# Performance work log

Hardware: AMD Instinct MI355X
Metric: run time of the kernel (lower is better)

Reference implementation:

```python
import jax, jax.numpy as jnp
import numpy as np

B, N, C, H = 4, 4096, 1024, 16
HD = C // H  # head_dim = 64
EPS = 1e-6


def setup_inputs() -> dict:
    key = jax.random.key(0)
    ks = jax.random.split(key, 5)
    x = jax.random.normal(ks[0], (B, N, C), dtype=jnp.float32)
    s_in = 1.0 / np.sqrt(C)
    W_qkv = jax.random.normal(ks[1], (C, 3 * C), dtype=jnp.float32) * s_in
    b_qkv = jnp.zeros((3 * C,), dtype=jnp.float32)
    W_out = jax.random.normal(ks[2], (C, C), dtype=jnp.float32) * s_in
    b_out = jnp.zeros((C,), dtype=jnp.float32)
    return {"x": x, "W_qkv": W_qkv, "b_qkv": b_qkv, "W_out": W_out, "b_out": b_out}


def reference(x, W_qkv, b_qkv, W_out, b_out):
    # qkv projection: (B, N, 3C)
    qkv = jnp.einsum('bnc,cf->bnf', x, W_qkv) + b_qkv
    # rearrange 'b n (h d) -> b h n d' with d = 3*head_dim, then chunk into q,k,v
    qkv = qkv.reshape(B, N, H, 3 * HD).transpose(0, 2, 1, 3)  # (B,H,N,3*HD)
    q, k, v = jnp.split(qkv, 3, axis=-1)  # each (B,H,N,HD)
    # silu feature map
    q = jax.nn.silu(q)
    k = jax.nn.silu(k)
    # linear attention: state = k^T @ v per head  -> (B,H,HD,HD)
    state = jnp.einsum('bhnd,bhne->bhde', k, v)
    k_sum = k.sum(axis=2)  # (B,H,HD)
    num = jnp.einsum('bhnd,bhde->bhne', q, state)  # (B,H,N,HD)
    den = jnp.einsum('bhnd,bhd->bhn', q, k_sum)[..., None]  # (B,H,N,1)
    out = num / (den + EPS)
    # 'b h n d -> b n (h d)'
    out = out.transpose(0, 2, 1, 3).reshape(B, N, C)
    return jnp.einsum('bnc,cf->bnf', out, W_out) + b_out
```

## Files before the change

kernel.cpp:

```cpp
#include <hip/hip_runtime.h>

typedef unsigned short u16;
typedef unsigned int u32;
typedef __attribute__((ext_vector_type(8))) short short8;
typedef __attribute__((ext_vector_type(8))) _Float16 half8;
typedef __attribute__((ext_vector_type(4))) float f32x4;

#define DEV __device__ __forceinline__

DEV void async_copy16(const void* g, void* l) {
  __builtin_amdgcn_global_load_lds((const __attribute__((address_space(1))) u32*)g,
                                   (__attribute__((address_space(3))) u32*)l, 16, 0, 0);
}
DEV float bf2f(u16 u) { return __uint_as_float(((u32)u) << 16); }
DEV u16 f2bf(float f) {
  u32 x = __float_as_uint(f);
  return (u16)((x + 0x7fffu + ((x >> 16) & 1u)) >> 16);
}
DEV u16 f2h_bits(float f) { _Float16 h = (_Float16)f; return __builtin_bit_cast(u16, h); }
DEV float h2f_bits(u16 b) { return (float)__builtin_bit_cast(_Float16, b); }
DEV float silu_f(float x) { return x / (1.0f + __expf(-x)); }

DEV void stage_tile(const u16* __restrict__ G, size_t grow_base, int k0, u16* L, int t) {
#pragma unroll
  for (int it = 0; it < 2; ++it) {
    int c = t + it * 256;
    int r = c >> 2, j = c & 3;
    int js = j ^ ((r >> 1) & 3);
    async_copy16(G + ((grow_base + (size_t)r) << 10) + k0 + js * 8,
                 (char*)L + (size_t)c * 16);
  }
}
DEV half8 frag(const u16* L, int rr, int lq) {
  int sw = lq ^ ((rr >> 1) & 3);
  return *(const half8*)((const char*)L + (size_t)rr * 64 + sw * 16);
}
DEV short8 frag_s(const u16* L, int rr, int lq) {
  int sw = lq ^ ((rr >> 1) & 3);
  return *(const short8*)((const char*)L + (size_t)rr * 64 + sw * 16);
}

__global__ __launch_bounds__(256) void transpose_k(const float* __restrict__ W,
                                                   u16* __restrict__ Wt,
                                                   int K, int N) {
  __shared__ float s[32][33];
  int t = threadIdx.x;
  int tx = t & 31, ty = t >> 5;
  int ntk = K >> 5;
  int bk = blockIdx.x % ntk, bn = blockIdx.x / ntk;
  int k0 = bk * 32, n0 = bn * 32;
#pragma unroll
  for (int i = 0; i < 4; ++i)
    s[ty + 8 * i][tx] = W[(size_t)(k0 + ty + 8 * i) * N + n0 + tx];
  __syncthreads();
#pragma unroll
  for (int i = 0; i < 4; ++i) {
    int r = ty + 8 * i;
    Wt[(size_t)(n0 + r) * K + k0 + tx] = f2bf(s[tx][r]);
  }
}

__global__ __launch_bounds__(256) void split_x(const float* __restrict__ x,
                                               u16* __restrict__ X0,
                                               u16* __restrict__ X1) {
  int i = (blockIdx.x * 256 + threadIdx.x) * 4;
  float4 v = *(const float4*)&x[i];
  ushort4 h0, h1;
  h0.x = f2h_bits(v.x); h1.x = f2h_bits((v.x - h2f_bits(h0.x)) * 4096.0f);
  h0.y = f2h_bits(v.y); h1.y = f2h_bits((v.y - h2f_bits(h0.y)) * 4096.0f);
  h0.z = f2h_bits(v.z); h1.z = f2h_bits((v.z - h2f_bits(h0.z)) * 4096.0f);
  h0.w = f2h_bits(v.w); h1.w = f2h_bits((v.w - h2f_bits(h0.w)) * 4096.0f);
  *(ushort4*)&X0[i] = h0;
  *(ushort4*)&X1[i] = h1;
}

__global__ __launch_bounds__(256) void split_w(const float* __restrict__ W,
                                               u16* __restrict__ W0t,
                                               u16* __restrict__ W1t) {
  __shared__ float s[32][33];
  int t = threadIdx.x;
  int tx = t & 31, ty = t >> 5;
  int bk = blockIdx.x & 31, bn = blockIdx.x >> 5;
  int k0 = bk * 32, n0 = bn * 32;
#pragma unroll
  for (int i = 0; i < 4; ++i)
    s[ty + 8 * i][tx] = W[(size_t)(k0 + ty + 8 * i) * 3072 + n0 + tx];
  __syncthreads();
#pragma unroll
  for (int i = 0; i < 4; ++i) {
    int r = ty + 8 * i;
    int col = n0 + r;
    int h = col / 192, rem = col - h * 192;
    int cty = rem >> 6, d = rem & 63;
    int pcol = cty * 1024 + h * 64 + d;
    float v = s[tx][r];
    u16 h0 = f2h_bits(v);
    u16 h1 = f2h_bits((v - h2f_bits(h0)) * 4096.0f);
    size_t o = (size_t)pcol * 1024 + k0 + tx;
    W0t[o] = h0;
    W1t[o] = h1;
  }
}

__global__ __launch_bounds__(256, 2) void gemm_qk_f16(
    const u16* __restrict__ X0, const u16* __restrict__ X1,
    const u16* __restrict__ W0, const u16* __restrict__ W1,
    const float* __restrict__ bq,
    float* __restrict__ Qf, float* __restrict__ Kf) {
  __shared__ u16 lA0[128 * 32];
  __shared__ u16 lA1[128 * 32];
  __shared__ u16 lB0[128 * 32];
  __shared__ u16 lB1[128 * 32];
  int t = threadIdx.x;
  int w = t >> 6, l = t & 63;
  int wr = w >> 1, wc = w & 1;
  int lr = l & 15, lq = l >> 4;
  int mb = blockIdx.y * 128, nb = blockIdx.x * 128;
  int cty = nb >> 10;
  f32x4 aM[4][4] = {};
  f32x4 aC[4][4] = {};

  for (int k0 = 0; k0 < 1024; k0 += 32) {
#pragma unroll
    for (int it = 0; it < 2; ++it) {
      int c = t + it * 256;
      int r = c >> 2, j = c & 3;
      int js = j ^ ((r >> 1) & 3);
      size_t goA = (((size_t)(mb + r)) << 10) + k0 + js * 8;
      size_t goB = (((size_t)(nb + r)) << 10) + k0 + js * 8;
      async_copy16(X0 + goA, (char*)lA0 + (size_t)c * 16);
      async_copy16(X1 + goA, (char*)lA1 + (size_t)c * 16);
      async_copy16(W0 + goB, (char*)lB0 + (size_t)c * 16);
      async_copy16(W1 + goB, (char*)lB1 + (size_t)c * 16);
    }
    __syncthreads();
    half8 b0[4], b1[4];
#pragma unroll
    for (int nn = 0; nn < 4; ++nn) {
      int rr = wc * 64 + nn * 16 + lr;
      b0[nn] = frag(lB0, rr, lq);
      b1[nn] = frag(lB1, rr, lq);
    }
#pragma unroll
    for (int m = 0; m < 4; ++m) {
      int rr = wr * 64 + m * 16 + lr;
      half8 a0 = frag(lA0, rr, lq);
      half8 a1 = frag(lA1, rr, lq);
#pragma unroll
      for (int nn = 0; nn < 4; ++nn) {
        aM[m][nn] = __builtin_amdgcn_mfma_f32_16x16x32_f16(a0, b0[nn], aM[m][nn], 0, 0, 0);
        aC[m][nn] = __builtin_amdgcn_mfma_f32_16x16x32_f16(a0, b1[nn], aC[m][nn], 0, 0, 0);
        aC[m][nn] = __builtin_amdgcn_mfma_f32_16x16x32_f16(a1, b0[nn], aC[m][nn], 0, 0, 0);
      }
    }
    __syncthreads();
  }

  const float cscale = 2.44140625e-4f;
  float* dst = (cty == 0) ? Qf : Kf;
#pragma unroll
  for (int nn = 0; nn < 4; ++nn) {
    int col = nb + wc * 64 + nn * 16 + lr;
    int h = (col & 1023) >> 6, d0 = col & 63;
    float bias = bq[h * 192 + cty * 64 + d0];
#pragma unroll
    for (int m = 0; m < 4; ++m)
#pragma unroll
      for (int j = 0; j < 4; ++j) {
        int row = mb + wr * 64 + m * 16 + lq * 4 + j;
        int b = row >> 12, n = row & 4095;
        size_t base = (((size_t)(b * 16 + h) * 4096 + n) << 6) + d0;
        float val = aM[m][nn][j] + aC[m][nn][j] * cscale + bias;
        dst[base] = silu_f(val);
      }
  }
}

__global__ __launch_bounds__(256) void gemm_v_f16(
    const u16* __restrict__ X0, const u16* __restrict__ W0,
    const float* __restrict__ bq, u16* __restrict__ Vb) {
  __shared__ u16 lA0[128 * 32];
  __shared__ u16 lB0[128 * 32];
  int t = threadIdx.x;
  int w = t >> 6, l = t & 63;
  int wr = w >> 1, wc = w & 1;
  int lr = l & 15, lq = l >> 4;
  int mb = blockIdx.y * 128, nb = 2048 + blockIdx.x * 128;
  f32x4 aM[4][4] = {};

  for (int k0 = 0; k0 < 1024; k0 += 32) {
    stage_tile(X0, mb, k0, lA0, t);
    stage_tile(W0, nb, k0, lB0, t);
    __syncthreads();
    half8 b0[4];
#pragma unroll
    for (int nn = 0; nn < 4; ++nn) b0[nn] = frag(lB0, wc * 64 + nn * 16 + lr, lq);
#pragma unroll
    for (int m = 0; m < 4; ++m) {
      half8 a0 = frag(lA0, wr * 64 + m * 16 + lr, lq);
#pragma unroll
      for (int nn = 0; nn < 4; ++nn)
        aM[m][nn] = __builtin_amdgcn_mfma_f32_16x16x32_f16(a0, b0[nn], aM[m][nn], 0, 0, 0);
    }
    __syncthreads();
  }
#pragma unroll
  for (int nn = 0; nn < 4; ++nn) {
    int col = nb + wc * 64 + nn * 16 + lr;
    int h = (col & 1023) >> 6, d0 = col & 63;
    float bias = bq[h * 192 + 128 + d0];
#pragma unroll
    for (int m = 0; m < 4; ++m)
#pragma unroll
      for (int j = 0; j < 4; ++j) {
        int row = mb + wr * 64 + m * 16 + lq * 4 + j;
        int b = row >> 12, n = row & 4095;
        size_t base = (((size_t)(b * 16 + h) * 4096 + n) << 6) + d0;
        Vb[base] = f2bf(aM[m][nn][j] + bias);
      }
  }
}

__global__ __launch_bounds__(256) void gemm_qkv(const float* __restrict__ X,
                                                const float* __restrict__ Wq,
                                                const float* __restrict__ bq,
                                                float* __restrict__ Qf,
                                                float* __restrict__ Kf,
                                                u16* __restrict__ Vb) {
  __shared__ float sA[16 * 132];
  __shared__ float sB[16 * 128];
  int t = threadIdx.x;
  int tm = t >> 4, tn = t & 15;
  int mb = blockIdx.y * 128, nb = blockIdx.x * 128;
  float acc[8][8] = {};

  for (int k0 = 0; k0 < 1024; k0 += 16) {
#pragma unroll
    for (int it = 0; it < 2; ++it) {
      int c = t + it * 256;
      int m = c >> 2, kc = (c & 3) * 4;
      float4 v = *(const float4*)&X[(size_t)(mb + m) * 1024 + k0 + kc];
      sA[(kc + 0) * 132 + m] = v.x;
      sA[(kc + 1) * 132 + m] = v.y;
      sA[(kc + 2) * 132 + m] = v.z;
      sA[(kc + 3) * 132 + m] = v.w;
      int kr = c >> 5, nc = (c & 31) * 4;
      async_copy16(&Wq[(size_t)(k0 + kr) * 3072 + nb + nc], (char*)sB + (size_t)c * 16);
    }
    __syncthreads();
#pragma unroll
    for (int k = 0; k < 16; ++k) {
      float4 a0 = *(const float4*)&sA[k * 132 + tm * 8];
      float4 a1 = *(const float4*)&sA[k * 132 + tm * 8 + 4];
      float4 b0 = *(const float4*)&sB[k * 128 + tn * 8];
      float4 b1 = *(const float4*)&sB[k * 128 + tn * 8 + 4];
      const float av[8] = {a0.x, a0.y, a0.z, a0.w, a1.x, a1.y, a1.z, a1.w};
      const float bv[8] = {b0.x, b0.y, b0.z, b0.w, b1.x, b1.y, b1.z, b1.w};
#pragma unroll
      for (int i = 0; i < 8; ++i)
#pragma unroll
        for (int j = 0; j < 8; ++j) acc[i][j] = fmaf(av[i], bv[j], acc[i][j]);
    }
    __syncthreads();
  }

  int c0 = nb + tn * 8;
  int h = c0 / 192, rem = c0 % 192;
  int ty = rem >> 6, d0 = rem & 63;
  float bb[8];
#pragma unroll
  for (int j = 0; j < 8; ++j) bb[j] = bq[c0 + j];
#pragma unroll
  for (int i = 0; i < 8; ++i) {
    int r = mb + tm * 8 + i;
    int b = r >> 12, n = r & 4095;
    size_t base = (((size_t)(b * 16 + h) * 4096 + n) << 6) + d0;
    if (ty == 2) {
      u16 pk[8];
#pragma unroll
      for (int j = 0; j < 8; ++j) pk[j] = f2bf(acc[i][j] + bb[j]);
      *(short8*)&Vb[base] = *(short8*)pk;
    } else {
      float* dst = (ty == 0) ? Qf : Kf;
#pragma unroll
      for (int j = 0; j < 8; ++j) dst[base + j] = silu_f(acc[i][j] + bb[j]);
    }
  }
}

__global__ __launch_bounds__(256) void state_partial(const float* __restrict__ Kf,
                                                     const u16* __restrict__ Vb,
                                                     float* __restrict__ stateP,
                                                     float* __restrict__ ksumP) {
  int bh = blockIdx.y, ch = blockIdx.x, t = threadIdx.x;
  __shared__ float sK[64 * 64];
  __shared__ u16 sV[64 * 64];
  __shared__ float sred[256];
  int n0 = ch * 512;
  size_t base = ((size_t)bh * 4096 + n0) << 6;
  float acc[4][4] = {};
  int te = t & 15, td = t >> 4;
  int kd = t & 63, kq = t >> 6;
  float kacc = 0.0f;

  for (int sc = 0; sc < 8; ++sc) {
    const float* gk = Kf + base + (size_t)sc * 64 * 64;
    const u16* gv = Vb + base + (size_t)sc * 64 * 64;
#pragma unroll
    for (int it = 0; it < 4; ++it)
      async_copy16(gk + (size_t)(t + it * 256) * 4, (char*)sK + (size_t)(t + it * 256) * 16);
#pragma unroll
    for (int it = 0; it < 2; ++it)
      async_copy16(gv + (size_t)(t + it * 256) * 8, (char*)sV + (size_t)(t + it * 256) * 16);
    __syncthreads();
#pragma unroll 4
    for (int n = 0; n < 64; ++n) {
      float4 k4 = *(const float4*)&sK[n * 64 + td * 4];
      const float ka[4] = {k4.x, k4.y, k4.z, k4.w};
      ushort4 vv = *(const ushort4*)&sV[n * 64 + te * 4];
      const float va[4] = {bf2f(vv.x), bf2f(vv.y), bf2f(vv.z), bf2f(vv.w)};
#pragma unroll
      for (int i = 0; i < 4; ++i)
#pragma unroll
        for (int j = 0; j < 4; ++j) acc[i][j] = fmaf(ka[i], va[j], acc[i][j]);
    }
#pragma unroll
    for (int i = 0; i < 16; ++i) kacc += sK[(kq * 16 + i) * 64 + kd];
    __syncthreads();
  }
  size_t pb = ((size_t)bh * 8 + ch) * 4096;
#pragma unroll
  for (int i = 0; i < 4; ++i)
#pragma unroll
    for (int j = 0; j < 4; ++j)
      stateP[pb + (size_t)(td * 4 + i) * 64 + te * 4 + j] = acc[i][j];

  sred[t] = kacc;
  __syncthreads();
  if (t < 64)
    ksumP[((size_t)bh * 8 + ch) * 64 + t] = sred[t] + sred[t + 64] + sred[t + 128] + sred[t + 192];
}

__global__ __launch_bounds__(256) void reduce_state(const float* __restrict__ stateP,
                                                    const float* __restrict__ ksumP,
                                                    float* __restrict__ stateF,
                                                    float* __restrict__ ksumF) {
  int bh = blockIdx.x, t = threadIdx.x;
#pragma unroll
  for (int i = 0; i < 16; ++i) {
    int e = t + i * 256;
    float s = 0.0f;
#pragma unroll
    for (int c = 0; c < 8; ++c) s += stateP[((size_t)bh * 8 + c) * 4096 + e];
    stateF[(size_t)bh * 4096 + e] = s;
  }
  if (t < 64) {
    float s = 0.0f;
#pragma unroll
    for (int c = 0; c < 8; ++c) s += ksumP[((size_t)bh * 8 + c) * 64 + t];
    ksumF[(size_t)bh * 64 + t] = s;
  }
}

__global__ __launch_bounds__(256) void attn_out(const float* __restrict__ Qf,
                                                const float* __restrict__ stateF,
                                                const float* __restrict__ ksumF,
                                                u16* __restrict__ outb) {
  int bh = blockIdx.y, chnk = blockIdx.x, t = threadIdx.x;
  __shared__ float sS[4096];
  __shared__ float sk[64];
#pragma unroll
  for (int i = 0; i < 16; ++i) {
    int e = t + i * 256;
    sS[e] = stateF[(size_t)bh * 4096 + e];
  }
  if (t < 64) sk[t] = ksumF[(size_t)bh * 64 + t];
  __syncthreads();

  int n = chnk * 256 + t;
  size_t qb = ((size_t)bh * 4096 + n) << 6;
  float4 a4[16] = {};
  float den = 0.0f;
#pragma unroll 4
  for (int dd = 0; dd < 16; ++dd) {
    float4 q4 = *(const float4*)&Qf[qb + dd * 4];
    const float qa[4] = {q4.x, q4.y, q4.z, q4.w};
#pragma unroll
    for (int jj = 0; jj < 4; ++jj) {
      int d = dd * 4 + jj;
      float qf = qa[jj];
      den = fmaf(qf, sk[d], den);
      const float4* srow = (const float4*)&sS[d * 64];
#pragma unroll
      for (int e4 = 0; e4 < 16; ++e4) {
        float4 s = srow[e4];
        a4[e4].x = fmaf(qf, s.x, a4[e4].x);
        a4[e4].y = fmaf(qf, s.y, a4[e4].y);
        a4[e4].z = fmaf(qf, s.z, a4[e4].z);
        a4[e4].w = fmaf(qf, s.w, a4[e4].w);
      }
    }
  }
  float rden = 1.0f / (den + 1e-6f);
  int b = bh >> 4, h = bh & 15;
  size_t ob = ((size_t)(b * 4096 + n) << 10) + h * 64;
#pragma unroll
  for (int e4 = 0; e4 < 16; ++e4) {
    ushort4 u;
    u.x = f2bf(a4[e4].x * rden);
    u.y = f2bf(a4[e4].y * rden);
    u.z = f2bf(a4[e4].z * rden);
    u.w = f2bf(a4[e4].w * rden);
    *(ushort4*)&outb[ob + e4 * 4] = u;
  }
}

__global__ __launch_bounds__(256) void gemm_out(const u16* __restrict__ A,
                                                const u16* __restrict__ Bt,
                                                const float* __restrict__ bias,
                                                float* __restrict__ C) {
  __shared__ u16 lA[128 * 32];
  __shared__ u16 lB[128 * 32];
  int t = threadIdx.x;
  int w = t >> 6, l = t & 63;
  int wr = w >> 1, wc = w & 1;
  int lr = l & 15, lq = l >> 4;
  int mb = blockIdx.y * 128, nb = blockIdx.x * 128;
  f32x4 acc[4][4] = {};

  for (int k0 = 0; k0 < 1024; k0 += 32) {
    stage_tile(A, mb, k0, lA, t);
    stage_tile(Bt, nb, k0, lB, t);
    __syncthreads();
    short8 af[4], bf[4];
#pragma unroll
    for (int m = 0; m < 4; ++m) af[m] = frag_s(lA, wr * 64 + m * 16 + lr, lq);
#pragma unroll
    for (int nn = 0; nn < 4; ++nn) bf[nn] = frag_s(lB, wc * 64 + nn * 16 + lr, lq);
#pragma unroll
    for (int m = 0; m < 4; ++m)
#pragma unroll
      for (int nn = 0; nn < 4; ++nn)
        acc[m][nn] = __builtin_amdgcn_mfma_f32_16x16x32_bf16(af[m], bf[nn], acc[m][nn], 0, 0, 0);
    __syncthreads();
  }

#pragma unroll
  for (int m = 0; m < 4; ++m)
#pragma unroll
    for (int nn = 0; nn < 4; ++nn) {
      int col = nb + wc * 64 + nn * 16 + lr;
      float bc = bias[col];
#pragma unroll
      for (int j = 0; j < 4; ++j) {
        int row = mb + wr * 64 + m * 16 + lq * 4 + j;
        C[((size_t)row << 10) + col] = acc[m][nn][j] + bc;
      }
    }
}

extern "C" void kernel_launch(void* const* d_in, const int* in_sizes, int n_in,
                              void* d_out, int out_size, void* d_ws, size_t ws_size,
                              hipStream_t stream) {
  const float* x    = (const float*)d_in[0];
  const float* Wqkv = (const float*)d_in[1];
  const float* bqkv = (const float*)d_in[2];
  const float* Wout = (const float*)d_in[3];
  const float* bout = (const float*)d_in[4];
  float* out = (float*)d_out;

  char* w = (char*)d_ws;
  const size_t offK  = 0;
  const size_t offV  = offK + 67108864ULL;
  const size_t offSP = offV + 33554432ULL;
  const size_t offKP = offSP + 8388608ULL;
  const size_t offWT = offKP + 131072ULL;
  const size_t offSF = offWT + 2097152ULL;
  const size_t offKF = offSF + 1048576ULL;
  const size_t need_base = offKF + 16384ULL;
  const size_t offX0 = need_base;
  const size_t offX1 = offX0 + 33554432ULL;
  const size_t offW0 = offX1 + 33554432ULL;
  const size_t offW1 = offW0 + 6291456ULL;
  const size_t need_fast = offW1 + 6291456ULL;

  if (ws_size < need_base) return;

  float* Kf     = (float*)(w + offK);
  u16*   outb   = (u16*)(w + offK);
  u16*   Vb     = (u16*)(w + offV);
  float* stateP = (float*)(w + offSP);
  float* ksumP  = (float*)(w + offKP);
  u16*   WoutT  = (u16*)(w + offWT);
  float* stateF = (float*)(w + offSF);
  float* ksumF  = (float*)(w + offKF);
  float* Qf     = out;

  transpose_k<<<dim3(1024), dim3(256), 0, stream>>>(Wout, WoutT, 1024, 1024);

  if (ws_size >= need_fast) {
    u16* X0 = (u16*)(w + offX0);
    u16* X1 = (u16*)(w + offX1);
    u16* W0 = (u16*)(w + offW0);
    u16* W1 = (u16*)(w + offW1);
    split_x<<<dim3(16384), dim3(256), 0, stream>>>(x, X0, X1);
    split_w<<<dim3(3072), dim3(256), 0, stream>>>(Wqkv, W0, W1);
    gemm_qk_f16<<<dim3(16, 128), dim3(256), 0, stream>>>(X0, X1, W0, W1, bqkv, Qf, Kf);
    gemm_v_f16<<<dim3(8, 128), dim3(256), 0, stream>>>(X0, W0, bqkv, Vb);
  } else {
    gemm_qkv<<<dim3(24, 128), dim3(256), 0, stream>>>(x, Wqkv, bqkv, Qf, Kf, Vb);
  }

  state_partial<<<dim3(8, 64), dim3(256), 0, stream>>>(Kf, Vb, stateP, ksumP);
  reduce_state<<<dim3(64), dim3(256), 0, stream>>>(stateP, ksumP, stateF, ksumF);
  attn_out<<<dim3(16, 64), dim3(256), 0, stream>>>(Qf, stateF, ksumF, outb);
  gemm_out<<<dim3(8, 128), dim3(256), 0, stream>>>(outb, WoutT, bout, out);
}
```

Before: 461.2 us.

## Use fp16 MFMA for Q·state attention output and fuse prep kernels

```diff
diff --git a/kernel.cpp b/kernel.cpp
--- a/kernel.cpp
+++ b/kernel.cpp
@@ -38,6 +38,9 @@
 DEV short8 frag_s(const u16* L, int rr, int lq) {
   int sw = lq ^ ((rr >> 1) & 3);
   return *(const short8*)((const char*)L + (size_t)rr * 64 + sw * 16);
+}
+DEV half8 frag64(const u16* L, int rr, int slot) {
+  return *(const half8*)(L + (size_t)rr * 64 + ((slot ^ (rr & 7)) * 8));
 }
 
 __global__ __launch_bounds__(256) void transpose_k(const float* __restrict__ W,
@@ -60,45 +63,61 @@
   }
 }
 
-__global__ __launch_bounds__(256) void split_x(const float* __restrict__ x,
-                                               u16* __restrict__ X0,
-                                               u16* __restrict__ X1) {
-  int i = (blockIdx.x * 256 + threadIdx.x) * 4;
-  float4 v = *(const float4*)&x[i];
-  ushort4 h0, h1;
-  h0.x = f2h_bits(v.x); h1.x = f2h_bits((v.x - h2f_bits(h0.x)) * 4096.0f);
-  h0.y = f2h_bits(v.y); h1.y = f2h_bits((v.y - h2f_bits(h0.y)) * 4096.0f);
-  h0.z = f2h_bits(v.z); h1.z = f2h_bits((v.z - h2f_bits(h0.z)) * 4096.0f);
-  h0.w = f2h_bits(v.w); h1.w = f2h_bits((v.w - h2f_bits(h0.w)) * 4096.0f);
-  *(ushort4*)&X0[i] = h0;
-  *(ushort4*)&X1[i] = h1;
-}
-
-__global__ __launch_bounds__(256) void split_w(const float* __restrict__ W,
-                                               u16* __restrict__ W0t,
-                                               u16* __restrict__ W1t) {
+__global__ __launch_bounds__(256) void prep(const float* __restrict__ x,
+                                            u16* __restrict__ X0, u16* __restrict__ X1,
+                                            const float* __restrict__ Wq,
+                                            u16* __restrict__ W0t, u16* __restrict__ W1t,
+                                            const float* __restrict__ Wo,
+                                            u16* __restrict__ WoT) {
   __shared__ float s[32][33];
-  int t = threadIdx.x;
-  int tx = t & 31, ty = t >> 5;
-  int bk = blockIdx.x & 31, bn = blockIdx.x >> 5;
-  int k0 = bk * 32, n0 = bn * 32;
-#pragma unroll
-  for (int i = 0; i < 4; ++i)
-    s[ty + 8 * i][tx] = W[(size_t)(k0 + ty + 8 * i) * 3072 + n0 + tx];
-  __syncthreads();
-#pragma unroll
-  for (int i = 0; i < 4; ++i) {
-    int r = ty + 8 * i;
-    int col = n0 + r;
-    int h = col / 192, rem = col - h * 192;
-    int cty = rem >> 6, d = rem & 63;
-    int pcol = cty * 1024 + h * 64 + d;
-    float v = s[tx][r];
-    u16 h0 = f2h_bits(v);
-    u16 h1 = f2h_bits((v - h2f_bits(h0)) * 4096.0f);
-    size_t o = (size_t)pcol * 1024 + k0 + tx;
-    W0t[o] = h0;
-    W1t[o] = h1;
+  int bid = blockIdx.x, t = threadIdx.x;
+  if (bid < 16384) {
+    int i = (bid * 256 + t) * 4;
+    float4 v = *(const float4*)&x[i];
+    ushort4 h0, h1;
+    h0.x = f2h_bits(v.x); h1.x = f2h_bits((v.x - h2f_bits(h0.x)) * 4096.0f);
+    h0.y = f2h_bits(v.y); h1.y = f2h_bits((v.y - h2f_bits(h0.y)) * 4096.0f);
+    h0.z = f2h_bits(v.z); h1.z = f2h_bits((v.z - h2f_bits(h0.z)) * 4096.0f);
+    h0.w = f2h_bits(v.w); h1.w = f2h_bits((v.w - h2f_bits(h0.w)) * 4096.0f);
+    *(ushort4*)&X0[i] = h0;
+    *(ushort4*)&X1[i] = h1;
+  } else if (bid < 16384 + 3072) {
+    int b2 = bid - 16384;
+    int tx = t & 31, ty = t >> 5;
+    int bk = b2 & 31, bn = b2 >> 5;
+    int k0 = bk * 32, n0 = bn * 32;
+#pragma unroll
+    for (int i = 0; i < 4; ++i)
+      s[ty + 8 * i][tx] = Wq[(size_t)(k0 + ty + 8 * i) * 3072 + n0 + tx];
+    __syncthreads();
+#pragma unroll
+    for (int i = 0; i < 4; ++i) {
+      int r = ty + 8 * i;
+      int col = n0 + r;
+      int h = col / 192, rem = col - h * 192;
+      int cty = rem >> 6, d = rem & 63;
+      int pcol = cty * 1024 + h * 64 + d;
+      float v = s[tx][r];
+      u16 h0 = f2h_bits(v);
+      u16 h1 = f2h_bits((v - h2f_bits(h0)) * 4096.0f);
+      size_t o = (size_t)pcol * 1024 + k0 + tx;
+      W0t[o] = h0;
+      W1t[o] = h1;
+    }
+  } else {
+    int b3 = bid - 19456;
+    int tx = t & 31, ty = t >> 5;
+    int bk = b3 & 31, bn = b3 >> 5;
+    int k0 = bk * 32, n0 = bn * 32;
+#pragma unroll
+    for (int i = 0; i < 4; ++i)
+      s[ty + 8 * i][tx] = Wo[(size_t)(k0 + ty + 8 * i) * 1024 + n0 + tx];
+    __syncthreads();
+#pragma unroll
+    for (int i = 0; i < 4; ++i) {
+      int r = ty + 8 * i;
+      WoT[(size_t)(n0 + r) * 1024 + k0 + tx] = f2bf(s[tx][r]);
+    }
   }
 }
 
@@ -343,16 +362,17 @@
 
 __global__ __launch_bounds__(256) void reduce_state(const float* __restrict__ stateP,
                                                     const float* __restrict__ ksumP,
-                                                    float* __restrict__ stateF,
+                                                    u16* __restrict__ sTh,
                                                     float* __restrict__ ksumF) {
   int bh = blockIdx.x, t = threadIdx.x;
 #pragma unroll
   for (int i = 0; i < 16; ++i) {
-    int e = t + i * 256;
+    int idx = t + i * 256;
     float s = 0.0f;
 #pragma unroll
-    for (int c = 0; c < 8; ++c) s += stateP[((size_t)bh * 8 + c) * 4096 + e];
-    stateF[(size_t)bh * 4096 + e] = s;
+    for (int c = 0; c < 8; ++c) s += stateP[((size_t)bh * 8 + c) * 4096 + idx];
+    int d = idx >> 6, e = idx & 63;
+    sTh[((size_t)bh << 12) + e * 64 + d] = f2h_bits(s);
   }
   if (t < 64) {
     float s = 0.0f;
@@ -362,56 +382,92 @@
   }
 }
 
-__global__ __launch_bounds__(256) void attn_out(const float* __restrict__ Qf,
-                                                const float* __restrict__ stateF,
-                                                const float* __restrict__ ksumF,
-                                                u16* __restrict__ outb) {
+__global__ __launch_bounds__(256) void attn_mfma(const float* __restrict__ Qf,
+                                                 const u16* __restrict__ sTh,
+                                                 const float* __restrict__ ksumF,
+                                                 u16* __restrict__ outb) {
+  __shared__ u16 q16[256 * 64];
+  __shared__ u16 sT[64 * 64];
+  __shared__ float denp[256 * 4];
+  __shared__ float den[256];
   int bh = blockIdx.y, chnk = blockIdx.x, t = threadIdx.x;
-  __shared__ float sS[4096];
-  __shared__ float sk[64];
-#pragma unroll
-  for (int i = 0; i < 16; ++i) {
-    int e = t + i * 256;
-    sS[e] = stateF[(size_t)bh * 4096 + e];
-  }
-  if (t < 64) sk[t] = ksumF[(size_t)bh * 64 + t];
+  int w = t >> 6, l = t & 63;
+  int lr16 = l & 15, lq4 = l >> 4;
+
+  {
+    const u16* src = sTh + ((size_t)bh << 12);
+#pragma unroll
+    for (int it = 0; it < 2; ++it) {
+      int c = t + it * 256;
+      short8 v = *(const short8*)(src + c * 8);
+      int e = c >> 3, slot = c & 7;
+      *(short8*)&sT[e * 64 + ((slot ^ (e & 7)) * 8)] = v;
+    }
+  }
+  {
+    int quarter = t & 3, rbase = t >> 2;
+    float4 skr[4];
+#pragma unroll
+    for (int i4 = 0; i4 < 4; ++i4)
+      skr[i4] = *(const float4*)&ksumF[(size_t)bh * 64 + quarter * 16 + i4 * 4];
+#pragma unroll
+    for (int p = 0; p < 4; ++p) {
+      int row = rbase + p * 64;
+      int n = chnk * 256 + row;
+      const float* qrow = Qf + (((size_t)bh * 4096 + n) << 6) + quarter * 16;
+      float dp = 0.0f;
+      u16 h[16];
+#pragma unroll
+      for (int i4 = 0; i4 < 4; ++i4) {
+        float4 v = *(const float4*)(qrow + i4 * 4);
+        dp += v.x * skr[i4].x + v.y * skr[i4].y + v.z * skr[i4].z + v.w * skr[i4].w;
+        h[i4 * 4 + 0] = f2h_bits(v.x);
+        h[i4 * 4 + 1] = f2h_bits(v.y);
+        h[i4 * 4 + 2] = f2h_bits(v.z);
+        h[i4 * 4 + 3] = f2h_bits(v.w);
+      }
+      denp[row * 4 + quarter] = dp;
+      int s0 = (quarter * 2) ^ (row & 7);
+      int s1 = (quarter * 2 + 1) ^ (row & 7);
+      *(short8*)&q16[row * 64 + s0 * 8] = *(short8*)&h[0];
+      *(short8*)&q16[row * 64 + s1 * 8] = *(short8*)&h[8];
+    }
+  }
   __syncthreads();
-
-  int n = chnk * 256 + t;
-  size_t qb = ((size_t)bh * 4096 + n) << 6;
-  float4 a4[16] = {};
-  float den = 0.0f;
-#pragma unroll 4
-  for (int dd = 0; dd < 16; ++dd) {
-    float4 q4 = *(const float4*)&Qf[qb + dd * 4];
-    const float qa[4] = {q4.x, q4.y, q4.z, q4.w};
-#pragma unroll
-    for (int jj = 0; jj < 4; ++jj) {
-      int d = dd * 4 + jj;
-      float qf = qa[jj];
-      den = fmaf(qf, sk[d], den);
-      const float4* srow = (const float4*)&sS[d * 64];
-#pragma unroll
-      for (int e4 = 0; e4 < 16; ++e4) {
-        float4 s = srow[e4];
-        a4[e4].x = fmaf(qf, s.x, a4[e4].x);
-        a4[e4].y = fmaf(qf, s.y, a4[e4].y);
-        a4[e4].z = fmaf(qf, s.z, a4[e4].z);
-        a4[e4].w = fmaf(qf, s.w, a4[e4].w);
+  den[t] = denp[t * 4] + denp[t * 4 + 1] + denp[t * 4 + 2] + denp[t * 4 + 3];
+  __syncthreads();
+
+  f32x4 acc[4][4] = {};
+#pragma unroll
+  for (int kh = 0; kh < 2; ++kh) {
+    half8 bfr[4];
+#pragma unroll
+    for (int nt = 0; nt < 4; ++nt)
+      bfr[nt] = frag64(sT, nt * 16 + lr16, kh * 4 + lq4);
+#pragma unroll
+    for (int rt = 0; rt < 4; ++rt) {
+      half8 a = frag64(q16, w * 64 + rt * 16 + lr16, kh * 4 + lq4);
+#pragma unroll
+      for (int nt = 0; nt < 4; ++nt)
+        acc[rt][nt] = __builtin_amdgcn_mfma_f32_16x16x32_f16(a, bfr[nt], acc[rt][nt], 0, 0, 0);
+    }
+  }
+
+  int b = bh >> 4, hh = bh & 15;
+#pragma unroll
+  for (int rt = 0; rt < 4; ++rt) {
+#pragma unroll
+    for (int j = 0; j < 4; ++j) {
+      int row = w * 64 + rt * 16 + lq4 * 4 + j;
+      float rden = 1.0f / (den[row] + 1e-6f);
+      int n = chnk * 256 + row;
+      size_t ob = (((size_t)(b * 4096 + n)) << 10) + hh * 64;
+#pragma unroll
+      for (int nt = 0; nt < 4; ++nt) {
+        int e = nt * 16 + lr16;
+        outb[ob + e] = f2bf(acc[rt][nt][j] * rden);
       }
     }
-  }
-  float rden = 1.0f / (den + 1e-6f);
-  int b = bh >> 4, h = bh & 15;
-  size_t ob = ((size_t)(b * 4096 + n) << 10) + h * 64;
-#pragma unroll
-  for (int e4 = 0; e4 < 16; ++e4) {
-    ushort4 u;
-    u.x = f2bf(a4[e4].x * rden);
-    u.y = f2bf(a4[e4].y * rden);
-    u.z = f2bf(a4[e4].z * rden);
-    u.w = f2bf(a4[e4].w * rden);
-    *(ushort4*)&outb[ob + e4 * 4] = u;
   }
 }
 
@@ -475,8 +531,8 @@
   const size_t offSP = offV + 33554432ULL;
   const size_t offKP = offSP + 8388608ULL;
   const size_t offWT = offKP + 131072ULL;
-  const size_t offSF = offWT + 2097152ULL;
-  const size_t offKF = offSF + 1048576ULL;
+  const size_t offST = offWT + 2097152ULL;
+  const size_t offKF = offST + 524288ULL;
   const size_t need_base = offKF + 16384ULL;
   const size_t offX0 = need_base;
   const size_t offX1 = offX0 + 33554432ULL;
@@ -492,27 +548,25 @@
   float* stateP = (float*)(w + offSP);
   float* ksumP  = (float*)(w + offKP);
   u16*   WoutT  = (u16*)(w + offWT);
-  float* stateF = (float*)(w + offSF);
+  u16*   sTh    = (u16*)(w + offST);
   float* ksumF  = (float*)(w + offKF);
   float* Qf     = out;
-
-  transpose_k<<<dim3(1024), dim3(256), 0, stream>>>(Wout, WoutT, 1024, 1024);
 
   if (ws_size >= need_fast) {
     u16* X0 = (u16*)(w + offX0);
     u16* X1 = (u16*)(w + offX1);
     u16* W0 = (u16*)(w + offW0);
     u16* W1 = (u16*)(w + offW1);
-    split_x<<<dim3(16384), dim3(256), 0, stream>>>(x, X0, X1);
-    split_w<<<dim3(3072), dim3(256), 0, stream>>>(Wqkv, W0, W1);
+    prep<<<dim3(20480), dim3(256), 0, stream>>>(x, X0, X1, Wqkv, W0, W1, Wout, WoutT);
     gemm_qk_f16<<<dim3(16, 128), dim3(256), 0, stream>>>(X0, X1, W0, W1, bqkv, Qf, Kf);
     gemm_v_f16<<<dim3(8, 128), dim3(256), 0, stream>>>(X0, W0, bqkv, Vb);
   } else {
+    transpose_k<<<dim3(1024), dim3(256), 0, stream>>>(Wout, WoutT, 1024, 1024);
     gemm_qkv<<<dim3(24, 128), dim3(256), 0, stream>>>(x, Wqkv, bqkv, Qf, Kf, Vb);
   }
 
   state_partial<<<dim3(8, 64), dim3(256), 0, stream>>>(Kf, Vb, stateP, ksumP);
-  reduce_state<<<dim3(64), dim3(256), 0, stream>>>(stateP, ksumP, stateF, ksumF);
-  attn_out<<<dim3(16, 64), dim3(256), 0, stream>>>(Qf, stateF, ksumF, outb);
+  reduce_state<<<dim3(64), dim3(256), 0, stream>>>(stateP, ksumP, sTh, ksumF);
+  attn_mfma<<<dim3(16, 64), dim3(256), 0, stream>>>(Qf, sTh, ksumF, outb);
   gemm_out<<<dim3(8, 128), dim3(256), 0, stream>>>(outb, WoutT, bout, out);
 }
```

New measurement: 433.0 us. 1.07x faster.
